# Kernel optimization log

Hardware: AMD Instinct MI355X
Metric: run time of the kernel (lower is better)

## Reference

```python
import jax, jax.numpy as jnp
import numpy as np

LN_EPS = 1e-5
DIM = 128
HEADS = 6
DIM_HEAD = 32
INNER = HEADS * DIM_HEAD          # 192
FF_INNER = int(DIM * 4 * 2 / 3)   # 341 (GEGLU inner dim)
LOCAL_WINDOW = 200
CACHE = 3
COMPRESS = 2
TW = LOCAL_WINDOW + CACHE         # 203
B = 2
T = 12800                         # 32 chunks of 400


def layer_norm(x, w, b):
    m = x.mean(-1, keepdims=True)
    v = ((x - m) ** 2).mean(-1, keepdims=True)
    return (x - m) / jnp.sqrt(v + LN_EPS) * w + b


def apply_rotary(q, k):
    # q, k: (b, h, n, d); standard half-rotation rotary over absolute positions
    d = q.shape[-1]
    n = q.shape[2]
    inv_freq = 1.0 / (10000.0 ** (jnp.arange(0, d, 2, dtype=jnp.float32) / d))
    freqs = jnp.arange(n, dtype=jnp.float32)[:, None] * inv_freq  # (n, d/2)
    emb = jnp.concatenate([freqs, freqs], axis=-1)                # (n, d)
    cos = jnp.cos(emb).astype(q.dtype)
    sin = jnp.sin(emb).astype(q.dtype)

    def rot_half(x):
        x1, x2 = jnp.split(x, 2, axis=-1)
        return jnp.concatenate([-x2, x1], axis=-1)

    rope = lambda x: x * cos + rot_half(x) * sin
    return rope(q), rope(k)


def local_attention(q, k, v, w):
    # causal local attention, look_backward=1 window, look_forward=0 (lucidrains LocalAttention)
    b, h, n, d = q.shape
    nw = n // w
    q, k = apply_rotary(q, k)
    qw = q.reshape(b, h, nw, w, d)

    def look_around(x):
        xw = x.reshape(b, h, nw, w, d)
        prev = jnp.pad(xw[:, :, :-1], ((0, 0), (0, 0), (1, 0), (0, 0), (0, 0)))
        return jnp.concatenate([prev, xw], axis=3)  # (b,h,nw,2w,d)

    kw = look_around(k)
    vw = look_around(v)

    t = jnp.arange(n).reshape(nw, w)
    tk_prev = jnp.pad(t[:-1], ((1, 0), (0, 0)), constant_values=-1)
    tk = jnp.concatenate([tk_prev, t], axis=1)  # (nw, 2w); -1 marks padding
    mask = (t[:, :, None] >= tk[:, None, :]) & (tk[:, None, :] >= 0)  # (nw, w, 2w)

    sim = jnp.einsum('bhwid,bhwjd->bhwij', qw, kw) * (d ** -0.5)
    neg = jnp.finfo(sim.dtype).min
    sim = jnp.where(mask[None, None], sim, neg)
    attn = jax.nn.softmax(sim, axis=-1)
    out = jnp.einsum('bhwij,bhwjd->bhwid', attn, vw)
    return out.reshape(b, h, n, d)


def local_mha(x, ln_w, ln_b, wqkv, wo, window):
    h = layer_norm(x, ln_w, ln_b)
    qkv = h @ wqkv                       # (b, n, 3*INNER)
    q, k, v = jnp.split(qkv, 3, axis=-1)

    def split_heads(t):
        bb, n, _ = t.shape
        return t.reshape(bb, n, HEADS, DIM_HEAD).transpose(0, 2, 1, 3)

    out = local_attention(split_heads(q), split_heads(k), split_heads(v), window)
    bb, hh, n, d = out.shape
    out = out.transpose(0, 2, 1, 3).reshape(bb, n, hh * d)
    return out @ wo


def feed_forward(x, ln_w, ln_b, w1, w2):
    h = layer_norm(x, ln_w, ln_b) @ w1   # (b, n, 2*FF_INNER)
    a, gate = jnp.split(h, 2, axis=-1)
    return (a * jax.nn.gelu(gate, approximate=False)) @ w2


def local_trans(x, ln1_w, ln1_b, wqkv, wo, ln2_w, ln2_b, w1, w2, window):
    n_layers = ln1_w.shape[0]
    for i in range(n_layers):
        x = x + local_mha(x, ln1_w[i], ln1_b[i], wqkv[i], wo[i], window)
        x = x + feed_forward(x, ln2_w[i], ln2_b[i], w1[i], w2[i])
    return x


def setup_inputs() -> dict:
    key = jax.random.key(0)
    ks = jax.random.split(key, 16)
    std = 0.02
    rn = lambda k, shape: jax.random.normal(k, shape, dtype=jnp.float32) * std
    inp = {
        'x': jax.random.normal(ks[0], (B, DIM, T), dtype=jnp.float32),
        'cache_token': jax.random.normal(ks[1], (1, CACHE * COMPRESS, DIM), dtype=jnp.float32),
    }
    ki = 2
    for g in ('dt', 'lt'):
        inp[g + '_ln1_w'] = jnp.ones((2, DIM), jnp.float32)
        inp[g + '_ln1_b'] = jnp.zeros((2, DIM), jnp.float32)
        inp[g + '_wqkv'] = rn(ks[ki], (2, DIM, 3 * INNER)); ki += 1
        inp[g + '_wo'] = rn(ks[ki], (2, INNER, DIM)); ki += 1
        inp[g + '_ln2_w'] = jnp.ones((2, DIM), jnp.float32)
        inp[g + '_ln2_b'] = jnp.zeros((2, DIM), jnp.float32)
        inp[g + '_w1'] = rn(ks[ki], (2, DIM, 2 * FF_INNER)); ki += 1
        inp[g + '_w2'] = rn(ks[ki], (2, FF_INNER, DIM)); ki += 1
    inp['conv_w'] = rn(ks[ki], (DIM, DIM, COMPRESS)); ki += 1
    inp['conv_b'] = jnp.zeros((DIM,), jnp.float32)
    return inp


def reference(x, cache_token,
              dt_ln1_w, dt_ln1_b, dt_wqkv, dt_wo, dt_ln2_w, dt_ln2_b, dt_w1, dt_w2,
              lt_ln1_w, lt_ln1_b, lt_wqkv, lt_wo, lt_ln2_w, lt_ln2_b, lt_w1, lt_w2,
              conv_w, conv_b):
    feat = x.transpose(0, 2, 1)                     # (B, T, C)
    b, t, c = feat.shape
    chunk = LOCAL_WINDOW * COMPRESS                 # 400
    nchunks = t // chunk
    feat = feat.reshape(b, nchunks, chunk, c)
    ct = jnp.broadcast_to(cache_token[:, None], (b, nchunks, CACHE * COMPRESS, c))
    feat = jnp.concatenate([ct, feat], axis=2)      # interleave cache tokens per chunk
    feat = feat.reshape(b, nchunks * (chunk + CACHE * COMPRESS), c)

    # DownTrans: 2-layer local transformer (window 406) + strided conv compress
    feat = local_trans(feat, dt_ln1_w, dt_ln1_b, dt_wqkv, dt_wo,
                       dt_ln2_w, dt_ln2_b, dt_w1, dt_w2, TW * COMPRESS)
    y = jax.lax.conv_general_dilated(
        feat.transpose(0, 2, 1), conv_w, (COMPRESS,), 'VALID',
        dimension_numbers=('NCH', 'OIH', 'NCH')) + conv_b[None, :, None]
    feat = y.transpose(0, 2, 1)                     # (B, n/2, C)

    # remaining depth-2 local transformer (window 203)
    feat = local_trans(feat, lt_ln1_w, lt_ln1_b, lt_wqkv, lt_wo,
                       lt_ln2_w, lt_ln2_b, lt_w1, lt_w2, TW)
    return feat
```

## Files before the change

kernel.cpp:

```cpp
#include <hip/hip_runtime.h>
#include <cstdint>
#include <cstddef>

#define DIM    128
#define HEADS  6
#define INNER  192
#define QKV3   576
#define FFI    341
#define FF2    682
#define GGP    352
#define BATCH  2
#define T_IN   12800
#define N1     12992
#define N2     6496
#define ROWS1  (BATCH * N1)
#define ROWS2  (BATCH * N2)
#define W_DT   406
#define W_LT   203

typedef unsigned short ushortT;
typedef unsigned int u32;
typedef __bf16 bf16x8 __attribute__((ext_vector_type(8)));
typedef float f32x4 __attribute__((ext_vector_type(4)));

__device__ __forceinline__ f32x4 mfma16(bf16x8 a, bf16x8 b, f32x4 c) {
  return __builtin_amdgcn_mfma_f32_16x16x32_bf16(a, b, c, 0, 0, 0);
}
__device__ __forceinline__ ushortT f2bf(float x) {
  union { __bf16 b; ushortT u; } c; c.b = (__bf16)x; return c.u;
}
__device__ __forceinline__ void async_copy16(const ushortT* g, ushortT* l) {
  __builtin_amdgcn_global_load_lds(
      (const __attribute__((address_space(1))) unsigned int*)g,
      (__attribute__((address_space(3))) unsigned int*)l, 16, 0, 0);
}

static constexpr size_t OF_FEAT = 0;
static constexpr size_t OF_H    = OF_FEAT + (size_t)ROWS1 * DIM;
static constexpr size_t OF_QKH  = OF_H + (size_t)ROWS1 * DIM / 2;
static constexpr size_t SZ_QKH  = ((size_t)(ROWS1 + 128) * 384) / 2;
static constexpr size_t OF_AO   = OF_QKH + SZ_QKH;
static constexpr size_t OF_VT   = OF_AO + (size_t)ROWS1 * INNER / 2;
static constexpr size_t SZ_VT   = ((size_t)384 * (N1 + 128)) / 2;
static constexpr size_t OF_GG   = OF_VT + SZ_VT;
static constexpr size_t OF_F2   = OF_GG + (size_t)ROWS1 * GGP / 2;
static constexpr size_t OF_WT   = OF_F2 + (size_t)ROWS2 * DIM;
static constexpr size_t WT_QKV = 0;
static constexpr size_t WT_WO  = 81920;
static constexpr size_t WT_W1  = 106496;
static constexpr size_t WT_W2  = 204800;
static constexpr size_t WT_SET = 249856;
static constexpr size_t OF_CW  = OF_WT + (4 * WT_SET) / 2 + 64;
static constexpr size_t OF_ROPE = OF_CW + (128 * 256) / 2 + 64;
static constexpr size_t OF_H2  = OF_ROPE + (size_t)N1 * 32;

__global__ void build_feat_kernel(const float* __restrict__ x,
                                  const float* __restrict__ cache,
                                  float* __restrict__ feat) {
  int idx = blockIdx.x * 256 + threadIdx.x;
  if (idx >= ROWS1 * DIM) return;
  int d = idx & 127;
  int row = idx >> 7;
  int b = row / N1;
  int i = row - b * N1;
  int c = i / 406;
  int j = i - c * 406;
  float v;
  if (j < 6) v = cache[j * DIM + d];
  else       v = x[((size_t)b * DIM + d) * T_IN + (c * 400 + j - 6)];
  feat[idx] = v;
}

__global__ __launch_bounds__(256) void ln_kernel(const float* __restrict__ x,
                                                 ushortT* __restrict__ y,
                                                 const float* __restrict__ w,
                                                 const float* __restrict__ bb,
                                                 int rows) {
  int row = blockIdx.x * 4 + (threadIdx.x >> 6);
  if (row >= rows) return;
  int lane = threadIdx.x & 63;
  const float* xr = x + (size_t)row * DIM;
  float2 v = *(const float2*)(xr + lane * 2);
  float s = v.x + v.y;
#pragma unroll
  for (int off = 32; off; off >>= 1) s += __shfl_xor(s, off);
  float mean = s * (1.0f / 128.0f);
  float dx = v.x - mean, dy = v.y - mean;
  float q = dx * dx + dy * dy;
#pragma unroll
  for (int off = 32; off; off >>= 1) q += __shfl_xor(q, off);
  float rstd = rsqrtf(q * (1.0f / 128.0f) + 1e-5f);
  float2 wv = *(const float2*)(w + lane * 2);
  float2 bv = *(const float2*)(bb + lane * 2);
  u32 packed = (u32)f2bf(dx * rstd * wv.x + bv.x) |
               ((u32)f2bf(dy * rstd * wv.y + bv.y) << 16);
  *(u32*)(y + (size_t)row * DIM + lane * 2) = packed;
}

__global__ __launch_bounds__(256) void gemm_nln(
    const ushortT* __restrict__ A, int lda,
    const ushortT* __restrict__ Wt, int ldw,
    const float* __restrict__ C, float* __restrict__ Co,
    const float* __restrict__ bias,
    int M, int Kpad, int addC,
    const float* __restrict__ lnw, const float* __restrict__ lnb,
    ushortT* __restrict__ hout, ushortT* __restrict__ bfout) {
  __shared__ ushortT As[64 * 32];
  __shared__ ushortT Bs[128 * 32];
  __shared__ float lnS[64][4];
  const int tid = threadIdx.x;
  const int wid = tid >> 6, lane = tid & 63;
  const int ck = lane & 15, quad = lane >> 4;
  const int bm = blockIdx.y * 64;
  const int wr = (wid >> 1) * 32, wc = (wid & 1) * 64;
  const int half = wid & 1;
  f32x4 acc[2][4];
#pragma unroll
  for (int t = 0; t < 2; t++)
#pragma unroll
    for (int u = 0; u < 4; u++) acc[t][u] = (f32x4){0.f, 0.f, 0.f, 0.f};

  for (int k0 = 0; k0 < Kpad; k0 += 32) {
    __syncthreads();
    {
      int idx = wid * 64 + lane;
      int row = idx >> 2, seg = (idx & 3) << 3;
      async_copy16(A + (size_t)(bm + row) * lda + k0 + seg, As + (size_t)(wid * 64) * 8);
    }
#pragma unroll
    for (int c2 = 0; c2 < 2; c2++) {
      int idx = c2 * 256 + wid * 64 + lane;
      int row = idx >> 2, seg = (idx & 3) << 3;
      async_copy16(Wt + (size_t)row * ldw + k0 + seg, Bs + (size_t)(c2 * 256 + wid * 64) * 8);
    }
    __syncthreads();
    bf16x8 af[2], bfr[4];
#pragma unroll
    for (int t = 0; t < 2; t++)
      af[t] = *(const bf16x8*)&As[(wr + t * 16 + ck) * 32 + quad * 8];
#pragma unroll
    for (int u = 0; u < 4; u++)
      bfr[u] = *(const bf16x8*)&Bs[(wc + u * 16 + ck) * 32 + quad * 8];
#pragma unroll
    for (int t = 0; t < 2; t++)
#pragma unroll
      for (int u = 0; u < 4; u++)
        acc[t][u] = mfma16(af[t], bfr[u], acc[t][u]);
  }

  float bv4[4] = {0.f, 0.f, 0.f, 0.f};
  if (bias) {
#pragma unroll
    for (int u = 0; u < 4; u++) bv4[u] = bias[wc + u * 16 + ck];
  }
  float res[2][4][4];
#pragma unroll
  for (int t = 0; t < 2; t++) {
#pragma unroll
    for (int r = 0; r < 4; r++) {
      int row = bm + wr + t * 16 + quad * 4 + r;
      const float* crow = C + (size_t)row * DIM;
#pragma unroll
      for (int u = 0; u < 4; u++) {
        int col = wc + u * 16 + ck;
        float v = acc[t][u][r] + bv4[u];
        if (addC) v += crow[col];
        res[t][r][u] = v;
      }
      if (Co) {
        float* orow = Co + (size_t)row * DIM;
#pragma unroll
        for (int u = 0; u < 4; u++) orow[wc + u * 16 + ck] = res[t][r][u];
      }
      if (bfout) {
        ushortT* brow = bfout + (size_t)row * DIM;
#pragma unroll
        for (int u = 0; u < 4; u++) brow[wc + u * 16 + ck] = f2bf(res[t][r][u]);
      }
    }
  }

  if (hout) {
#pragma unroll
    for (int t = 0; t < 2; t++) {
#pragma unroll
      for (int r = 0; r < 4; r++) {
        float s1 = ((res[t][r][0] + res[t][r][1]) + (res[t][r][2] + res[t][r][3]));
        float s2 = ((res[t][r][0] * res[t][r][0] + res[t][r][1] * res[t][r][1]) +
                    (res[t][r][2] * res[t][r][2] + res[t][r][3] * res[t][r][3]));
        s1 += __shfl_xor(s1, 1); s2 += __shfl_xor(s2, 1);
        s1 += __shfl_xor(s1, 2); s2 += __shfl_xor(s2, 2);
        s1 += __shfl_xor(s1, 4); s2 += __shfl_xor(s2, 4);
        s1 += __shfl_xor(s1, 8); s2 += __shfl_xor(s2, 8);
        if (ck == 0) {
          int rowIn = wr + t * 16 + quad * 4 + r;
          lnS[rowIn][half * 2]     = s1;
          lnS[rowIn][half * 2 + 1] = s2;
        }
      }
    }
    __syncthreads();
    float lw[4], lb[4];
#pragma unroll
    for (int u = 0; u < 4; u++) {
      lw[u] = lnw[wc + u * 16 + ck];
      lb[u] = lnb[wc + u * 16 + ck];
    }
#pragma unroll
    for (int t = 0; t < 2; t++) {
#pragma unroll
      for (int r = 0; r < 4; r++) {
        int rowIn = wr + t * 16 + quad * 4 + r;
        float S1 = lnS[rowIn][0] + lnS[rowIn][2];
        float S2 = lnS[rowIn][1] + lnS[rowIn][3];
        float mean = S1 * (1.0f / 128.0f);
        float var = S2 * (1.0f / 128.0f) - mean * mean;
        float rstd = rsqrtf(var + 1e-5f);
        ushortT* hrow = hout + (size_t)(bm + rowIn) * DIM;
#pragma unroll
        for (int u = 0; u < 4; u++) {
          int col = wc + u * 16 + ck;
          hrow[col] = f2bf((res[t][r][u] - mean) * rstd * lw[u] + lb[u]);
        }
      }
    }
  }
}

__global__ __launch_bounds__(256) void gemm_qkv(
    const ushortT* __restrict__ A,
    const ushortT* __restrict__ Wt,
    const float2* __restrict__ rope,
    ushortT* __restrict__ qkh,
    ushortT* __restrict__ vt,
    int M, int nseq, int nseqP) {
  __shared__ ushortT As[128 * 32];
  __shared__ ushortT Bs[128 * 32];
  const int tid = threadIdx.x;
  const int wid = tid >> 6, lane = tid & 63;
  const int ck = lane & 15, quad = lane >> 4;
  const int bm = blockIdx.y * 128, bn = blockIdx.x * 128;
  const int wr = (wid >> 1) * 64, wc = (wid & 1) * 64;
  f32x4 acc[4][4];
#pragma unroll
  for (int t = 0; t < 4; t++)
#pragma unroll
    for (int u = 0; u < 4; u++) acc[t][u] = (f32x4){0.f, 0.f, 0.f, 0.f};

  for (int k0 = 0; k0 < 128; k0 += 32) {
    __syncthreads();
#pragma unroll
    for (int c2 = 0; c2 < 2; c2++) {
      int idx = c2 * 256 + wid * 64 + lane;
      int row = idx >> 2, seg = (idx & 3) << 3;
      int ar = bm + row; if (ar > M - 1) ar = M - 1;
      async_copy16(A + (size_t)ar * 128 + k0 + seg, As + (size_t)(c2 * 256 + wid * 64) * 8);
      async_copy16(Wt + (size_t)(bn + row) * 128 + k0 + seg, Bs + (size_t)(c2 * 256 + wid * 64) * 8);
    }
    __syncthreads();
    bf16x8 af[4], bfr[4];
#pragma unroll
    for (int t = 0; t < 4; t++)
      af[t] = *(const bf16x8*)&As[(wr + t * 16 + ck) * 32 + quad * 8];
#pragma unroll
    for (int u = 0; u < 4; u++)
      bfr[u] = *(const bf16x8*)&Bs[(wc + u * 16 + ck) * 32 + quad * 8];
#pragma unroll
    for (int t = 0; t < 4; t++)
#pragma unroll
      for (int u = 0; u < 4; u++)
        acc[t][u] = mfma16(af[t], bfr[u], acc[t][u]);
  }

  const int s = bn + wc;
  if (s >= QKV3) return;

  if (s < 384) {
    const bool isQ = s < 192;
    const float SCq = 0.17677669529663687f * 1.4426950408889634f;
#pragma unroll
    for (int t = 0; t < 4; t++) {
#pragma unroll
      for (int r = 0; r < 4; r++) {
        int row = bm + wr + t * 16 + quad * 4 + r;
        if (row >= M) continue;
        int pos = (row >= nseq) ? row - nseq : row;
        float2 cssn = rope[pos * 16 + ck];
        float cs = cssn.x, sn = cssn.y;
        ushortT* orow = qkh + (size_t)row * 384;
#pragma unroll
        for (int u = 0; u < 4; u += 2) {
          float a0 = acc[t][u][r], a1 = acc[t][u + 1][r];
          float o0 = a0 * cs - a1 * sn;
          float o1 = a1 * cs + a0 * sn;
          if (isQ) { o0 *= SCq; o1 *= SCq; }
          int c0 = s + u * 16 + ck;
          orow[c0]      = f2bf(o0);
          orow[c0 + 16] = f2bf(o1);
        }
      }
    }
  } else {
#pragma unroll
    for (int t = 0; t < 4; t++) {
      int rowb = bm + wr + t * 16 + quad * 4;
      if (rowb >= M) continue;
      int bb = (rowb >= nseq) ? 1 : 0;
      int posb = rowb - bb * nseq;
#pragma unroll
      for (int u = 0; u < 4; u++) {
        int cv = s - 384 + u * 16 + ck;
        int hh = cv >> 5, d = cv & 31;
        ushort4 o;
        o.x = f2bf(acc[t][u][0]);
        o.y = f2bf(acc[t][u][1]);
        o.z = f2bf(acc[t][u][2]);
        o.w = f2bf(acc[t][u][3]);
        *(ushort4*)(vt + ((size_t)((bb * 6 + hh) * 32 + d)) * nseqP + posb) = o;
      }
    }
  }
}

__global__ __launch_bounds__(256) void gemm_w1g(
    const ushortT* __restrict__ A,
    const ushortT* __restrict__ Wt,
    ushortT* __restrict__ gg,
    int M) {
  __shared__ ushortT As[128 * 32];
  __shared__ ushortT Bs[128 * 32];
  const int tid = threadIdx.x;
  const int wid = tid >> 6, lane = tid & 63;
  const int ck = lane & 15, quad = lane >> 4;
  const int bm = blockIdx.y * 128, bn = blockIdx.x * 128;
  const int wr = (wid >> 1) * 64, wc = (wid & 1) * 64;
  f32x4 acc[4][4];
#pragma unroll
  for (int t = 0; t < 4; t++)
#pragma unroll
    for (int u = 0; u < 4; u++) acc[t][u] = (f32x4){0.f, 0.f, 0.f, 0.f};

  for (int k0 = 0; k0 < 128; k0 += 32) {
    __syncthreads();
#pragma unroll
    for (int c2 = 0; c2 < 2; c2++) {
      int idx = c2 * 256 + wid * 64 + lane;
      int row = idx >> 2, seg = (idx & 3) << 3;
      int ar = bm + row; if (ar > M - 1) ar = M - 1;
      async_copy16(A + (size_t)ar * 128 + k0 + seg, As + (size_t)(c2 * 256 + wid * 64) * 8);
      async_copy16(Wt + (size_t)(bn + row) * 128 + k0 + seg, Bs + (size_t)(c2 * 256 + wid * 64) * 8);
    }
    __syncthreads();
    bf16x8 af[4], bfr[4];
#pragma unroll
    for (int t = 0; t < 4; t++)
      af[t] = *(const bf16x8*)&As[(wr + t * 16 + ck) * 32 + quad * 8];
#pragma unroll
    for (int u = 0; u < 4; u++)
      bfr[u] = *(const bf16x8*)&Bs[(wc + u * 16 + ck) * 32 + quad * 8];
#pragma unroll
    for (int t = 0; t < 4; t++)
#pragma unroll
      for (int u = 0; u < 4; u++)
        acc[t][u] = mfma16(af[t], bfr[u], acc[t][u]);
  }

  const int s = bn + wc;
  if (s >= 704) return;
#pragma unroll
  for (int t = 0; t < 4; t++) {
#pragma unroll
    for (int r = 0; r < 4; r++) {
      int row = bm + wr + t * 16 + quad * 4 + r;
      if (row >= M) continue;
      ushortT* orow = gg + (size_t)row * GGP;
#pragma unroll
      for (int u = 0; u < 4; u += 2) {
        float a  = acc[t][u][r];
        float gt = acc[t][u + 1][r];
        float ge = 0.5f * gt * (1.0f + erff(gt * 0.70710678118654752f));
        int p = ((s + u * 16) >> 5) * 16 + ck;
        orow[p] = f2bf(a * ge);
      }
    }
  }
}

__global__ __launch_bounds__(256) void attn_kernel(
    const ushortT* __restrict__ qkh, const ushortT* __restrict__ vt,
    ushortT* __restrict__ out, int nseq, int nseqP, int w, int nw, int qgroups) {
  __shared__ ushortT Ks[64 * 32];
  __shared__ ushortT Vs[32 * 64];
  __shared__ ushortT Ps[4 * 16 * 72];

  const int bx = blockIdx.x;
  const int c = bx % nw;
  const int g = (qgroups - 1) - bx / nw;
  const int h = blockIdx.y;
  const int b = blockIdx.z;
  const int tid = threadIdx.x;
  const int wv = tid >> 6;
  const int lane = tid & 63;
  const int ck = lane & 15;
  const int quad = lane >> 4;

  const ushortT* gq = qkh + (size_t)b * nseq * 384;
  const ushortT* gv = vt + ((size_t)(b * 6 + h) * 32) * nseqP;
  const int cw = c * w;
  const int q0 = g * 64;
  const int qt = q0 + wv * 16;
  const bool wave_on = qt < w;

  const int j0 = (c > 0) ? (c - 1) * w : 0;
  const int jend_block = cw + min(q0 + 63, w - 1) + 1;
  const int jend_wave = wave_on ? (cw + min(qt + 15, w - 1) + 1) : 0;

  bf16x8 qf;
  {
    int qrow = cw + min(qt + ck, w - 1);
    qf = *(const bf16x8*)(gq + (size_t)qrow * 384 + h * 32 + quad * 8);
  }

  const int dstSlot = tid ^ ((tid >> 3) & 7);
  const int krow = tid >> 2, kch = tid & 3;
  const ushortT* ksrc = gq + (size_t)krow * 384 + 192 + h * 32 + kch * 8;
  const int vd = tid >> 3, vks = tid & 7;
  const ushortT* vsrc = gv + (size_t)vd * nseqP + vks * 8;

  const int p0 = (8 * ck + quad) ^ (ck & 7);
  const int p1 = (8 * ck + quad + 4) ^ (ck & 7);

  f32x4 olo = {0.f, 0.f, 0.f, 0.f};
  f32x4 ohi = {0.f, 0.f, 0.f, 0.f};
  float lp[4] = {0.f, 0.f, 0.f, 0.f};
  ushortT* pw = Ps + wv * 16 * 72;

  float4 kreg = *(const float4*)(ksrc + (size_t)j0 * 384);
  float4 vreg = *(const float4*)(vsrc + j0);

  for (int tb = j0; tb < jend_block; tb += 64) {
    __syncthreads();
    *(float4*)&Ks[(size_t)dstSlot * 8] = kreg;
    *(float4*)&Vs[(size_t)dstSlot * 8] = vreg;
    __syncthreads();
    if (tb + 64 < jend_block) {
      kreg = *(const float4*)(ksrc + (size_t)(tb + 64) * 384);
      vreg = *(const float4*)(vsrc + tb + 64);
    }
    if (tb < jend_wave) {
      bf16x8 kf0 = *(const bf16x8*)&Ks[p0 * 8];
      bf16x8 kf1 = *(const bf16x8*)&Ks[p1 * 8];
      bf16x8 kf2 = *(const bf16x8*)&Ks[p0 * 8 + 1024];
      bf16x8 kf3 = *(const bf16x8*)&Ks[p1 * 8 + 1024];
      f32x4 z = {0.f, 0.f, 0.f, 0.f};
      f32x4 s0 = mfma16(qf, kf0, z);
      f32x4 s1 = mfma16(qf, kf1, z);
      f32x4 s2 = mfma16(qf, kf2, z);
      f32x4 s3 = mfma16(qf, kf3, z);
      if (tb + 63 > cw + qt) {
        int key0 = tb + 2 * ck;
#pragma unroll
        for (int r = 0; r < 4; r++) {
          int qg = cw + qt + quad * 4 + r;
          if (key0 > qg)      s0[r] = -__builtin_inff();
          if (key0 + 1 > qg)  s1[r] = -__builtin_inff();
          if (key0 + 32 > qg) s2[r] = -__builtin_inff();
          if (key0 + 33 > qg) s3[r] = -__builtin_inff();
        }
      }
#pragma unroll
      for (int r = 0; r < 4; r++) {
        float pp0 = exp2f(s0[r]);
        float pp1 = exp2f(s1[r]);
        float pp2 = exp2f(s2[r]);
        float pp3 = exp2f(s3[r]);
        lp[r] += (pp0 + pp1) + (pp2 + pp3);
        int row72 = (quad * 4 + r) * 72;
        *(u32*)&pw[row72 + 2 * ck]      = (u32)f2bf(pp0) | ((u32)f2bf(pp1) << 16);
        *(u32*)&pw[row72 + 32 + 2 * ck] = (u32)f2bf(pp2) | ((u32)f2bf(pp3) << 16);
      }
      bf16x8 pf0 = *(const bf16x8*)&pw[ck * 72 + quad * 8];
      bf16x8 pf1 = *(const bf16x8*)&pw[ck * 72 + 32 + quad * 8];
      bf16x8 vlo0 = *(const bf16x8*)&Vs[p0 * 8];
      bf16x8 vlo1 = *(const bf16x8*)&Vs[p1 * 8];
      bf16x8 vhi0 = *(const bf16x8*)&Vs[p0 * 8 + 1024];
      bf16x8 vhi1 = *(const bf16x8*)&Vs[p1 * 8 + 1024];
      olo = mfma16(pf0, vlo0, olo);
      olo = mfma16(pf1, vlo1, olo);
      ohi = mfma16(pf0, vhi0, ohi);
      ohi = mfma16(pf1, vhi1, ohi);
    }
  }

  if (wave_on) {
#pragma unroll
    for (int r = 0; r < 4; r++) {
      float lr = lp[r];
      lr += __shfl_xor(lr, 1);
      lr += __shfl_xor(lr, 2);
      lr += __shfl_xor(lr, 4);
      lr += __shfl_xor(lr, 8);
      int qi = qt + quad * 4 + r;
      if (qi < w) {
        float inv = 1.0f / lr;
        ushortT* orow = out + ((size_t)b * nseq + cw + qi) * INNER + h * 32;
        orow[ck]      = f2bf(olo[r] * inv);
        orow[ck + 16] = f2bf(ohi[r] * inv);
      }
    }
  }
}

__global__ void wconvert_all_kernel(
    const float* __restrict__ dq, const float* __restrict__ dwo,
    const float* __restrict__ dw1, const float* __restrict__ dw2,
    const float* __restrict__ lq, const float* __restrict__ lwo,
    const float* __restrict__ lw1, const float* __restrict__ lw2,
    const float* __restrict__ convw,
    ushortT* __restrict__ wt, ushortT* __restrict__ cwt,
    float2* __restrict__ rope) {
  int idx = blockIdx.x * 256 + threadIdx.x;
  const int TOTW = 4 * (int)WT_SET;
  const int CWN = 128 * 256;
  if (idx < TOTW) {
    int s = idx / (int)WT_SET;
    int rem = idx - s * (int)WT_SET;
    int lyr = s & 1;
    const float* Wq = ((s < 2) ? dq : lq) + (size_t)lyr * DIM * QKV3;
    const float* Wo = ((s < 2) ? dwo : lwo) + (size_t)lyr * INNER * DIM;
    const float* W1 = ((s < 2) ? dw1 : lw1) + (size_t)lyr * DIM * FF2;
    const float* W2 = ((s < 2) ? dw2 : lw2) + (size_t)lyr * FFI * DIM;
    float v = 0.f;
    if (rem < (int)WT_WO) {
      int n = rem >> 7, k = rem & 127;
      if (n < QKV3) v = Wq[(size_t)k * QKV3 + n];
    } else if (rem < (int)WT_W1) {
      int r = rem - (int)WT_WO;
      int n = r / INNER, k = r - n * INNER;
      v = Wo[(size_t)k * DIM + n];
    } else if (rem < (int)WT_W2) {
      int r = rem - (int)WT_W1;
      int n = r >> 7, k = r & 127;
      if (n < 704) {
        int blk = n >> 5, wi = n & 31;
        int p = blk * 16 + (wi & 15);
        if (p < FFI) {
          int src = (wi < 16) ? p : FFI + p;
          v = W1[(size_t)k * FF2 + src];
        }
      }
    } else {
      int r = rem - (int)WT_W2;
      int n = r / GGP, k = r - n * GGP;
      if (k < FFI) v = W2[(size_t)k * DIM + n];
    }
    wt[idx] = f2bf(v);
  } else if (idx < TOTW + CWN) {
    int r = idx - TOTW;
    int o = r >> 8, k = r & 255;
    int kk = k >> 7, i = k & 127;
    cwt[r] = f2bf(convw[((size_t)o * DIM + i) * 2 + kk]);
  } else {
    int r = idx - TOTW - CWN;
    if (r < N1 * 16) {
      int pos = r >> 4, k = r & 15;
      float invf = 1.0f / powf(10000.0f, (float)k * (1.0f / 16.0f));
      float sn, cs;
      sincosf((float)pos * invf, &sn, &cs);
      rope[r] = make_float2(cs, sn);
    }
  }
}

static void run_layer(float* F, float* Fout, ushortT* hbuf, ushortT* qkh, ushortT* vtb,
                      ushortT* attnb, ushortT* ggb, const ushortT* wt,
                      const float2* rope,
                      int M, int nseq, int w,
                      const float* ln2w, const float* ln2b,
                      const float* nlnw, const float* nlnb,
                      ushortT* w2bf, hipStream_t stream) {
  int nseqP = nseq + 128;
  int gy = (M + 127) / 128;
  int gy64 = M / 64;
  gemm_qkv<<<dim3(5, gy), 256, 0, stream>>>(hbuf, wt + WT_QKV, rope, qkh, vtb, M, nseq, nseqP);
  int nw = nseq / w;
  int qgroups = (w + 63) / 64;
  attn_kernel<<<dim3(nw * qgroups, HEADS, BATCH), 256, 0, stream>>>(qkh, vtb, attnb,
                                                                    nseq, nseqP, w, nw, qgroups);
  gemm_nln<<<dim3(1, gy64), 256, 0, stream>>>(attnb, INNER, wt + WT_WO, INNER, F, F,
                                              nullptr, M, INNER, 1, ln2w, ln2b,
                                              hbuf, nullptr);
  gemm_w1g<<<dim3(6, gy), 256, 0, stream>>>(hbuf, wt + WT_W1, ggb, M);
  gemm_nln<<<dim3(1, gy64), 256, 0, stream>>>(ggb, GGP, wt + WT_W2, GGP, F, Fout,
                                              nullptr, M, GGP, 1, nlnw, nlnb,
                                              nlnw ? hbuf : (ushortT*)nullptr, w2bf);
}

extern "C" void kernel_launch(void* const* d_in, const int* in_sizes, int n_in,
                              void* d_out, int out_size, void* d_ws, size_t ws_size,
                              hipStream_t stream) {
  const float* x        = (const float*)d_in[0];
  const float* cache    = (const float*)d_in[1];
  const float* dt_ln1_w = (const float*)d_in[2];
  const float* dt_ln1_b = (const float*)d_in[3];
  const float* dt_wqkv  = (const float*)d_in[4];
  const float* dt_wo    = (const float*)d_in[5];
  const float* dt_ln2_w = (const float*)d_in[6];
  const float* dt_ln2_b = (const float*)d_in[7];
  const float* dt_w1    = (const float*)d_in[8];
  const float* dt_w2    = (const float*)d_in[9];
  const float* lt_ln1_w = (const float*)d_in[10];
  const float* lt_ln1_b = (const float*)d_in[11];
  const float* lt_wqkv  = (const float*)d_in[12];
  const float* lt_wo    = (const float*)d_in[13];
  const float* lt_ln2_w = (const float*)d_in[14];
  const float* lt_ln2_b = (const float*)d_in[15];
  const float* lt_w1    = (const float*)d_in[16];
  const float* lt_w2    = (const float*)d_in[17];
  const float* conv_w   = (const float*)d_in[18];
  const float* conv_b   = (const float*)d_in[19];

  float* ws     = (float*)d_ws;
  float* feat   = ws + OF_FEAT;
  ushortT* h    = (ushortT*)(ws + OF_H);
  ushortT* qkh  = (ushortT*)(ws + OF_QKH);
  ushortT* attnb= (ushortT*)(ws + OF_AO);
  ushortT* vtb  = (ushortT*)(ws + OF_VT);
  ushortT* ggb  = (ushortT*)(ws + OF_GG);
  float* feat2  = ws + OF_F2;
  ushortT* wt   = (ushortT*)(ws + OF_WT);
  ushortT* cwt  = (ushortT*)(ws + OF_CW);
  float2* rope  = (float2*)(ws + OF_ROPE);
  ushortT* h2   = (ushortT*)(ws + OF_H2);
  float* outf   = (float*)d_out;

  {
    int total = 4 * (int)WT_SET + 128 * 256 + N1 * 16;
    wconvert_all_kernel<<<(total + 255) / 256, 256, 0, stream>>>(
        dt_wqkv, dt_wo, dt_w1, dt_w2, lt_wqkv, lt_wo, lt_w1, lt_w2,
        conv_w, wt, cwt, rope);
  }

  build_feat_kernel<<<(ROWS1 * DIM + 255) / 256, 256, 0, stream>>>(x, cache, feat);
  ln_kernel<<<ROWS1 / 4, 256, 0, stream>>>(feat, h, dt_ln1_w, dt_ln1_b, ROWS1);

  run_layer(feat, feat, h, qkh, vtb, attnb, ggb, wt + 0 * WT_SET, rope,
            ROWS1, N1, W_DT,
            dt_ln2_w, dt_ln2_b, dt_ln1_w + DIM, dt_ln1_b + DIM, nullptr, stream);
  run_layer(feat, nullptr, h, qkh, vtb, attnb, ggb, wt + 1 * WT_SET, rope,
            ROWS1, N1, W_DT,
            dt_ln2_w + DIM, dt_ln2_b + DIM, nullptr, nullptr, h, stream);

  gemm_nln<<<dim3(1, ROWS2 / 64), 256, 0, stream>>>(h, 256, cwt, 256,
                                                    feat2, feat2, conv_b,
                                                    ROWS2, 256, 0,
                                                    lt_ln1_w, lt_ln1_b, h2, nullptr);

  run_layer(feat2, feat2, h2, qkh, vtb, attnb, ggb, wt + 2 * WT_SET, rope,
            ROWS2, N2, W_LT,
            lt_ln2_w, lt_ln2_b, lt_ln1_w + DIM, lt_ln1_b + DIM, nullptr, stream);
  run_layer(feat2, outf, h2, qkh, vtb, attnb, ggb, wt + 3 * WT_SET, rope,
            ROWS2, N2, W_LT,
            lt_ln2_w + DIM, lt_ln2_b + DIM, nullptr, nullptr, nullptr, stream);
}
```

Baseline: 548.9 us.

## Keep attention probabilities in registers via transposed QK and double-buffer K/V tiles

The QK^T MFMA is computed transposed (K as A operand, Q as B operand), so the exp'd probabilities land in registers already in the layout needed as the A operand of the PV MFMA. This removes the per-tile LDS round trip through the P scratch buffer. K is stored with a permuted row swizzle to match the new layout. K and V shared tiles are double-buffered, which drops one __syncthreads per iteration while prefetching the next tile. The row-sum reduction becomes a per-lane sum followed by a cross-quad shuffle.

```diff
diff --git a/kernel.cpp b/kernel.cpp
--- a/kernel.cpp
+++ b/kernel.cpp
@@ -389,9 +389,8 @@
 __global__ __launch_bounds__(256) void attn_kernel(
     const ushortT* __restrict__ qkh, const ushortT* __restrict__ vt,
     ushortT* __restrict__ out, int nseq, int nseqP, int w, int nw, int qgroups) {
-  __shared__ ushortT Ks[64 * 32];
-  __shared__ ushortT Vs[32 * 64];
-  __shared__ ushortT Ps[4 * 16 * 72];
+  __shared__ __align__(16) ushortT Ks[2][64 * 32];
+  __shared__ __align__(16) ushortT Vs[2][32 * 64];
 
   const int bx = blockIdx.x;
   const int c = bx % nw;
@@ -414,6 +413,7 @@
   const int j0 = (c > 0) ? (c - 1) * w : 0;
   const int jend_block = cw + min(q0 + 63, w - 1) + 1;
   const int jend_wave = wave_on ? (cw + min(qt + 15, w - 1) + 1) : 0;
+  const int ntiles = (jend_block - j0 + 63) >> 6;
 
   bf16x8 qf;
   {
@@ -421,91 +421,108 @@
     qf = *(const bf16x8*)(gq + (size_t)qrow * 384 + h * 32 + quad * 8);
   }
 
-  const int dstSlot = tid ^ ((tid >> 3) & 7);
   const int krow = tid >> 2, kch = tid & 3;
+  const int krho = ((krow >> 5) << 5) | (((krow >> 2) & 1) << 4) |
+                   (((krow >> 3) & 3) << 2) | (krow & 3);
+  const int kslot = krho * 4 + kch;
+  const int kphys = kslot ^ ((kslot >> 3) & 7);
   const ushortT* ksrc = gq + (size_t)krow * 384 + 192 + h * 32 + kch * 8;
-  const int vd = tid >> 3, vks = tid & 7;
-  const ushortT* vsrc = gv + (size_t)vd * nseqP + vks * 8;
-
-  const int p0 = (8 * ck + quad) ^ (ck & 7);
-  const int p1 = (8 * ck + quad + 4) ^ (ck & 7);
+  const int vphys = tid ^ ((tid >> 3) & 7);
+  const ushortT* vsrc = gv + (size_t)(tid >> 3) * nseqP + (tid & 7) * 8;
+
+  const int kbase = ((4 * ck + quad) ^ (ck >> 1)) * 8;
+  const int p0 = ((8 * ck + quad) ^ (ck & 7)) * 8;
+  const int p1 = ((8 * ck + quad + 4) ^ (ck & 7)) * 8;
 
   f32x4 olo = {0.f, 0.f, 0.f, 0.f};
   f32x4 ohi = {0.f, 0.f, 0.f, 0.f};
-  float lp[4] = {0.f, 0.f, 0.f, 0.f};
-  ushortT* pw = Ps + wv * 16 * 72;
-
-  float4 kreg = *(const float4*)(ksrc + (size_t)j0 * 384);
-  float4 vreg = *(const float4*)(vsrc + j0);
-
-  for (int tb = j0; tb < jend_block; tb += 64) {
-    __syncthreads();
-    *(float4*)&Ks[(size_t)dstSlot * 8] = kreg;
-    *(float4*)&Vs[(size_t)dstSlot * 8] = vreg;
-    __syncthreads();
-    if (tb + 64 < jend_block) {
-      kreg = *(const float4*)(ksrc + (size_t)(tb + 64) * 384);
-      vreg = *(const float4*)(vsrc + tb + 64);
+  float lsum = 0.f;
+
+  float4 kreg, vreg;
+  {
+    kreg = *(const float4*)(ksrc + (size_t)j0 * 384);
+    vreg = *(const float4*)(vsrc + j0);
+    *(float4*)&Ks[0][(size_t)kphys * 8] = kreg;
+    *(float4*)&Vs[0][(size_t)vphys * 8] = vreg;
+    int t1 = j0 + 64 * min(1, ntiles - 1);
+    kreg = *(const float4*)(ksrc + (size_t)t1 * 384);
+    vreg = *(const float4*)(vsrc + t1);
+  }
+
+  for (int tbi = 0; tbi < ntiles; tbi++) {
+    const int tb = j0 + (tbi << 6);
+    __syncthreads();
+    {
+      int bsel = (tbi + 1) & 1;
+      *(float4*)&Ks[bsel][(size_t)kphys * 8] = kreg;
+      *(float4*)&Vs[bsel][(size_t)vphys * 8] = vreg;
+    }
+    {
+      int tn = j0 + 64 * min(tbi + 2, ntiles - 1);
+      kreg = *(const float4*)(ksrc + (size_t)tn * 384);
+      vreg = *(const float4*)(vsrc + tn);
     }
     if (tb < jend_wave) {
-      bf16x8 kf0 = *(const bf16x8*)&Ks[p0 * 8];
-      bf16x8 kf1 = *(const bf16x8*)&Ks[p1 * 8];
-      bf16x8 kf2 = *(const bf16x8*)&Ks[p0 * 8 + 1024];
-      bf16x8 kf3 = *(const bf16x8*)&Ks[p1 * 8 + 1024];
+      const ushortT* KsB = Ks[tbi & 1];
+      const ushortT* VsB = Vs[tbi & 1];
+      bf16x8 kf0 = *(const bf16x8*)&KsB[kbase];
+      bf16x8 kf1 = *(const bf16x8*)&KsB[kbase + 512];
+      bf16x8 kf2 = *(const bf16x8*)&KsB[kbase + 1024];
+      bf16x8 kf3 = *(const bf16x8*)&KsB[kbase + 1536];
+      bf16x8 vlo0 = *(const bf16x8*)&VsB[p0];
+      bf16x8 vlo1 = *(const bf16x8*)&VsB[p1];
+      bf16x8 vhi0 = *(const bf16x8*)&VsB[p0 + 1024];
+      bf16x8 vhi1 = *(const bf16x8*)&VsB[p1 + 1024];
       f32x4 z = {0.f, 0.f, 0.f, 0.f};
-      f32x4 s0 = mfma16(qf, kf0, z);
-      f32x4 s1 = mfma16(qf, kf1, z);
-      f32x4 s2 = mfma16(qf, kf2, z);
-      f32x4 s3 = mfma16(qf, kf3, z);
+      f32x4 s0 = mfma16(kf0, qf, z);
+      f32x4 s1 = mfma16(kf1, qf, z);
+      f32x4 s2 = mfma16(kf2, qf, z);
+      f32x4 s3 = mfma16(kf3, qf, z);
       if (tb + 63 > cw + qt) {
-        int key0 = tb + 2 * ck;
+        int q = cw + qt + ck;
+        int kb = tb + 8 * quad;
 #pragma unroll
         for (int r = 0; r < 4; r++) {
-          int qg = cw + qt + quad * 4 + r;
-          if (key0 > qg)      s0[r] = -__builtin_inff();
-          if (key0 + 1 > qg)  s1[r] = -__builtin_inff();
-          if (key0 + 32 > qg) s2[r] = -__builtin_inff();
-          if (key0 + 33 > qg) s3[r] = -__builtin_inff();
+          if (kb + r > q)      s0[r] = -__builtin_inff();
+          if (kb + 4 + r > q)  s1[r] = -__builtin_inff();
+          if (kb + 32 + r > q) s2[r] = -__builtin_inff();
+          if (kb + 36 + r > q) s3[r] = -__builtin_inff();
         }
       }
-#pragma unroll
-      for (int r = 0; r < 4; r++) {
-        float pp0 = exp2f(s0[r]);
-        float pp1 = exp2f(s1[r]);
-        float pp2 = exp2f(s2[r]);
-        float pp3 = exp2f(s3[r]);
-        lp[r] += (pp0 + pp1) + (pp2 + pp3);
-        int row72 = (quad * 4 + r) * 72;
-        *(u32*)&pw[row72 + 2 * ck]      = (u32)f2bf(pp0) | ((u32)f2bf(pp1) << 16);
-        *(u32*)&pw[row72 + 32 + 2 * ck] = (u32)f2bf(pp2) | ((u32)f2bf(pp3) << 16);
-      }
-      bf16x8 pf0 = *(const bf16x8*)&pw[ck * 72 + quad * 8];
-      bf16x8 pf1 = *(const bf16x8*)&pw[ck * 72 + 32 + quad * 8];
-      bf16x8 vlo0 = *(const bf16x8*)&Vs[p0 * 8];
-      bf16x8 vlo1 = *(const bf16x8*)&Vs[p1 * 8];
-      bf16x8 vhi0 = *(const bf16x8*)&Vs[p0 * 8 + 1024];
-      bf16x8 vhi1 = *(const bf16x8*)&Vs[p1 * 8 + 1024];
-      olo = mfma16(pf0, vlo0, olo);
-      olo = mfma16(pf1, vlo1, olo);
-      ohi = mfma16(pf0, vhi0, ohi);
-      ohi = mfma16(pf1, vhi1, ohi);
-    }
-  }
-
+      float e00 = exp2f(s0[0]), e01 = exp2f(s0[1]), e02 = exp2f(s0[2]), e03 = exp2f(s0[3]);
+      float e10 = exp2f(s1[0]), e11 = exp2f(s1[1]), e12 = exp2f(s1[2]), e13 = exp2f(s1[3]);
+      float e20 = exp2f(s2[0]), e21 = exp2f(s2[1]), e22 = exp2f(s2[2]), e23 = exp2f(s2[3]);
+      float e30 = exp2f(s3[0]), e31 = exp2f(s3[1]), e32 = exp2f(s3[2]), e33 = exp2f(s3[3]);
+      lsum += (((e00 + e01) + (e02 + e03)) + ((e10 + e11) + (e12 + e13))) +
+              (((e20 + e21) + (e22 + e23)) + ((e30 + e31) + (e32 + e33)));
+      union { bf16x8 v; u32 u[4]; } pa0, pa1;
+      pa0.u[0] = (u32)f2bf(e00) | ((u32)f2bf(e01) << 16);
+      pa0.u[1] = (u32)f2bf(e02) | ((u32)f2bf(e03) << 16);
+      pa0.u[2] = (u32)f2bf(e10) | ((u32)f2bf(e11) << 16);
+      pa0.u[3] = (u32)f2bf(e12) | ((u32)f2bf(e13) << 16);
+      pa1.u[0] = (u32)f2bf(e20) | ((u32)f2bf(e21) << 16);
+      pa1.u[1] = (u32)f2bf(e22) | ((u32)f2bf(e23) << 16);
+      pa1.u[2] = (u32)f2bf(e30) | ((u32)f2bf(e31) << 16);
+      pa1.u[3] = (u32)f2bf(e32) | ((u32)f2bf(e33) << 16);
+      olo = mfma16(pa0.v, vlo0, olo);
+      olo = mfma16(pa1.v, vlo1, olo);
+      ohi = mfma16(pa0.v, vhi0, ohi);
+      ohi = mfma16(pa1.v, vhi1, ohi);
+    }
+  }
+
+  lsum += __shfl_xor(lsum, 16);
+  lsum += __shfl_xor(lsum, 32);
+  float inv = 1.0f / lsum;
   if (wave_on) {
 #pragma unroll
     for (int r = 0; r < 4; r++) {
-      float lr = lp[r];
-      lr += __shfl_xor(lr, 1);
-      lr += __shfl_xor(lr, 2);
-      lr += __shfl_xor(lr, 4);
-      lr += __shfl_xor(lr, 8);
+      float invr = __shfl(inv, quad * 4 + r);
       int qi = qt + quad * 4 + r;
       if (qi < w) {
-        float inv = 1.0f / lr;
         ushortT* orow = out + ((size_t)b * nseq + cw + qi) * INNER + h * 32;
-        orow[ck]      = f2bf(olo[r] * inv);
-        orow[ck + 16] = f2bf(ohi[r] * inv);
+        orow[ck]      = f2bf(olo[r] * invr);
+        orow[ck + 16] = f2bf(ohi[r] * invr);
       }
     }
   }
```

Result: no change. 550.4 us (+0.3%).
